# Kernel optimization log

Measured on AMD Instinct MI355X. Metric: run time of the kernel, lower is better.

Reference implementation:

```python
import jax, jax.numpy as jnp
import numpy as np

SEQ = 2048
D_MODEL = 2048
N_HEAD = 16
D_QK = 128
D_V = 128


def setup_inputs() -> dict:
    key = jax.random.key(0)
    ks = jax.random.split(key, 5)
    return {
        "x": jax.random.normal(ks[0], (SEQ, D_MODEL), dtype=jnp.float32),
        "q": jax.random.normal(ks[1], (N_HEAD, D_MODEL, D_QK), dtype=jnp.float32),
        "k": jax.random.normal(ks[2], (N_HEAD, D_MODEL, D_QK), dtype=jnp.float32),
        "v": jax.random.normal(ks[3], (N_HEAD, D_MODEL, D_V), dtype=jnp.float32),
        "o": jax.random.normal(ks[4], (N_HEAD, D_V, D_MODEL), dtype=jnp.float32),
        "theta_factor": jnp.asarray(10000.0, dtype=jnp.float32),
    }


def _rope_embed(x, theta_factor, d_qk):
    # x: [n_head, seq, d_qk]; faithful to source: rate is LINEAR in theta_factor
    seq = x.shape[1]
    d_rope = d_qk // 2
    rate = theta_factor * (-jnp.arange(d_rope, dtype=x.dtype) / d_rope)  # [d_rope]
    pos = jnp.arange(seq, dtype=x.dtype)                                 # [seq]
    rot = pos[:, None] * rate[None, :]                                   # [seq, d_rope]
    sin, cos = jnp.sin(rot), jnp.cos(rot)
    x1, x2 = x[..., :d_rope], x[..., d_rope:]
    y = jnp.concatenate([cos * x1 - sin * x2, sin * x1 + cos * x2], axis=-1)
    return y / d_qk ** 0.25  # qk_layer_norm is None path


def reference(x, q, k, v, o, theta_factor):
    seq, d_model = x.shape
    n_head, _, d_qk = q.shape
    d_v = v.shape[2]
    scale = 1.0 / jnp.sqrt(jnp.asarray(n_head * d_v * d_model, dtype=x.dtype))
    # causal mask: (tril - 1) * 1e9, as in source
    mask = (jnp.tril(jnp.ones((seq, seq), dtype=x.dtype)) - 1.0) * 1e9
    # per-head projections (vmapped heads expressed as einsum over h)
    rq = _rope_embed(jnp.einsum('sd,hde->hse', x, q), theta_factor, d_qk)
    rk = _rope_embed(jnp.einsum('sd,hde->hse', x, k), theta_factor, d_qk)
    vs = jnp.einsum('sd,hdv->hsv', x, v)
    scores = jnp.einsum('hse,hte->hst', rq, rk) + mask  # [h, s, s]
    w = jax.nn.softmax(scores, axis=-1)
    y = jnp.einsum('hst,htv->hsv', w, vs)
    z = jnp.einsum('hsv,hvd->sd', y, o)
    return z * scale
```

## Files before the change

kernel.cpp:

```cpp
#include <hip/hip_runtime.h>
#include <math.h>


typedef _Float16 half_t;
typedef __attribute__((ext_vector_type(8))) _Float16 half8;
typedef __attribute__((ext_vector_type(4))) float f32x4;

#define SEQ   2048
#define DM    2048
#define NHEAD 16

__device__ __forceinline__ f32x4 mfma16(half8 a, half8 b, f32x4 c) {
  return __builtin_amdgcn_mfma_f32_16x16x32_f16(a, b, c, 0, 0, 0);
}

__device__ __forceinline__ void gll16(const half_t* g, half_t* l) {
  __builtin_amdgcn_global_load_lds(
      (const __attribute__((address_space(1))) unsigned int*)g,
      (__attribute__((address_space(3))) unsigned int*)l, 16, 0, 0);
}

template <int CTRL>
__device__ __forceinline__ float dppf(float v) {
  int r = __builtin_amdgcn_mov_dpp(__builtin_bit_cast(int, v), CTRL, 0xF, 0xF,
                                   true);
  return __builtin_bit_cast(float, r);
}
__device__ __forceinline__ float red16_max(float v) {
  v = fmaxf(v, dppf<0xB1>(v));
  v = fmaxf(v, dppf<0x4E>(v));
  v = fmaxf(v, dppf<0x141>(v));
  v = fmaxf(v, dppf<0x140>(v));
  return v;
}
__device__ __forceinline__ float red16_sum(float v) {
  v += dppf<0xB1>(v);
  v += dppf<0x4E>(v);
  v += dppf<0x141>(v);
  v += dppf<0x140>(v);
  return v;
}

__device__ __forceinline__ void tpose32(const float* __restrict__ in,
                                        half_t* __restrict__ hi,
                                        half_t* __restrict__ lo, int R, int C,
                                        int r0, int c0, float (*tile)[33],
                                        int tid) {
  int tx = tid & 31, ty = tid >> 5;
#pragma unroll
  for (int i = 0; i < 32; i += 8)
    tile[ty + i][tx] = in[(size_t)(r0 + ty + i) * C + c0 + tx];
  __syncthreads();
#pragma unroll
  for (int i = 0; i < 32; i += 8) {
    float v = tile[tx][ty + i];
    half_t h = (half_t)v;
    size_t oidx = (size_t)(c0 + ty + i) * R + r0 + tx;
    hi[oidx] = h;
    if (lo) lo[oidx] = (half_t)(v - (float)h);
  }
}

__global__ __launch_bounds__(256)
void k_pre(const float* __restrict__ x, const float* __restrict__ q,
           const float* __restrict__ k, const float* __restrict__ v,
           const float* __restrict__ o, const float* __restrict__ thetap,
           half_t* __restrict__ Xh, half_t* __restrict__ Xl,
           half_t* __restrict__ WTh, half_t* __restrict__ WTl,
           half_t* __restrict__ VhT, half_t* __restrict__ OT,
           float2* __restrict__ trig) {
  __shared__ float tile[32][33];
  int b = blockIdx.x, tid = threadIdx.x;
  if (b < 4096) {
    int i = b * 256 + tid;
    float4 vv = ((const float4*)x)[i];
    union { half_t h[4]; uint2 u; } H, L;
    H.h[0] = (half_t)vv.x; H.h[1] = (half_t)vv.y;
    H.h[2] = (half_t)vv.z; H.h[3] = (half_t)vv.w;
    L.h[0] = (half_t)(vv.x - (float)H.h[0]);
    L.h[1] = (half_t)(vv.y - (float)H.h[1]);
    L.h[2] = (half_t)(vv.z - (float)H.h[2]);
    L.h[3] = (half_t)(vv.w - (float)H.h[3]);
    *(uint2*)&Xh[(size_t)i * 4] = H.u;
    *(uint2*)&Xl[(size_t)i * 4] = L.u;
  } else if (b < 16384) {
    int j = b - 4096;
    int which = j >> 12, z = (j >> 8) & 15, tb = j & 255;
    int c0 = (tb & 3) * 32, r0 = (tb >> 2) * 32;
    const float* src =
        (which == 0 ? q : which == 1 ? k : v) + (size_t)z * 2048 * 128;
    size_t doff = (size_t)z * 128 * 2048;
    if (which == 0)
      tpose32(src, WTh + doff, WTl + doff, 2048, 128, r0, c0, tile, tid);
    else if (which == 1) {
      size_t koff = (size_t)16 * 128 * 2048 + doff;
      tpose32(src, WTh + koff, WTl + koff, 2048, 128, r0, c0, tile, tid);
    } else
      tpose32(src, VhT + doff, nullptr, 2048, 128, r0, c0, tile, tid);
  } else if (b < 20480) {
    int j = b - 16384;
    int c0 = (j & 63) * 32, r0 = (j >> 6) * 32;
    tpose32(o, OT, nullptr, 2048, 2048, r0, c0, tile, tid);
  } else {
    int idx = (b - 20480) * 256 + tid;
    int s = idx >> 6, e = idx & 63;
    float th = thetap[0];
    float rate = th * (-(float)e * (1.0f / 64.0f));
    float rot = (float)s * rate;
    double rev = (double)rot * 0.15915494309189535;
    double fr = rev - rint(rev);
    float thr = (float)(fr * 6.283185307179586);
    float sn = sinf(thr), cs = cosf(thr);
    const float inv4 = 0.2973017787506803f;
    trig[idx] = make_float2(cs * inv4, sn * inv4);
  }
}

__global__ __launch_bounds__(256, 2)
void k_proj(const half_t* __restrict__ Xh, const half_t* __restrict__ Xl,
            const half_t* __restrict__ WTh, const half_t* __restrict__ WTl,
            const float2* __restrict__ trig, half_t* __restrict__ Rh,
            half_t* __restrict__ Rl) {
  __shared__ __align__(16) char smem[65536];
  half_t* sAh = (half_t*)smem;
  half_t* sAl = (half_t*)(smem + 16384);
  half_t* sBh = (half_t*)(smem + 32768);
  half_t* sBl = (half_t*)(smem + 49152);
  int y = blockIdx.y;
  int m0 = blockIdx.x * 128;
  const half_t* wth = WTh + (size_t)y * 128 * DM;
  const half_t* wtl = WTl + (size_t)y * 128 * DM;
  int lane = threadIdx.x & 63, wave = threadIdx.x >> 6;
  int l15 = lane & 15, quad = lane >> 4;
  int wm = wave >> 1, wn = wave & 1;

  f32x4 acc[4][4];
#pragma unroll
  for (int a = 0; a < 4; ++a)
#pragma unroll
    for (int b = 0; b < 4; ++b) acc[a][b] = (f32x4)0.0f;

  for (int kt = 0; kt < DM / 64; ++kt) {
    int k0 = kt * 64;
#pragma unroll
    for (int i = 0; i < 4; ++i) {
      int c = wave * 4 + i;
      int g = c * 64 + lane;
      int row = g >> 3;
      int lc = (g & 7) ^ (row & 7);
      size_t ro = (size_t)row * DM + k0 + lc * 8;
      gll16(Xh + (size_t)m0 * DM + ro, sAh + c * 512);
      gll16(Xl + (size_t)m0 * DM + ro, sAl + c * 512);
      gll16(wth + ro, sBh + c * 512);
      gll16(wtl + ro, sBl + c * 512);
    }
    __syncthreads();
#pragma unroll
    for (int kk = 0; kk < 2; ++kk) {
      half8 ah[4], al[4], bh[4], bl[4];
#pragma unroll
      for (int t = 0; t < 4; ++t) {
        int ar = wm * 64 + t * 16 + l15;
        int br = wn * 64 + t * 16 + l15;
        int ao = ar * 64 + (((kk * 4 + quad) ^ (ar & 7)) * 8);
        int bo = br * 64 + (((kk * 4 + quad) ^ (br & 7)) * 8);
        ah[t] = *(const half8*)&sAh[ao];
        al[t] = *(const half8*)&sAl[ao];
        bh[t] = *(const half8*)&sBh[bo];
        bl[t] = *(const half8*)&sBl[bo];
      }
#pragma unroll
      for (int im = 0; im < 4; ++im)
#pragma unroll
        for (int in = 0; in < 4; ++in) {
          acc[im][in] = mfma16(ah[im], bh[in], acc[im][in]);
          acc[im][in] = mfma16(ah[im], bl[in], acc[im][in]);
          acc[im][in] = mfma16(al[im], bh[in], acc[im][in]);
        }
    }
    __syncthreads();
  }
  float* tile = (float*)smem;
  size_t ybase = (size_t)y * SEQ * 128;
#pragma unroll
  for (int p = 0; p < 2; ++p) {
    if (p) __syncthreads();
    if (wm == p) {
#pragma unroll
      for (int im = 0; im < 4; ++im)
#pragma unroll
        for (int in = 0; in < 4; ++in)
#pragma unroll
          for (int r = 0; r < 4; ++r)
            tile[(im * 16 + quad * 4 + r) * 132 + wn * 64 + in * 16 + l15] =
                acc[im][in][r];
    }
    __syncthreads();
    int e = lane;
#pragma unroll 4
    for (int rr = 0; rr < 16; ++rr) {
      int rloc = wave * 16 + rr;
      int s = m0 + p * 64 + rloc;
      float x1 = tile[rloc * 132 + e];
      float x2 = tile[rloc * 132 + 64 + e];
      float2 sc = trig[s * 64 + e];
      float y1 = sc.x * x1 - sc.y * x2;
      float y2 = sc.y * x1 + sc.x * x2;
      half_t h1 = (half_t)y1, h2 = (half_t)y2;
      size_t base = ybase + (size_t)s * 128;
      Rh[base + e] = h1;       Rl[base + e] = (half_t)(y1 - (float)h1);
      Rh[base + 64 + e] = h2;  Rl[base + 64 + e] = (half_t)(y2 - (float)h2);
    }
  }
}

template <int HALF_OUT>
__global__ __launch_bounds__(256)
void k_gemm1(const half_t* __restrict__ A, const half_t* __restrict__ B,
             void* __restrict__ Cv, float scale) {
  __shared__ __align__(16) half_t sA[64 * 64], sB[128 * 64];
  int lin = blockIdx.y * 16 + blockIdx.x;
  int xcd = lin & 7, slot = lin >> 3;
  int bx = (xcd & 3) * 4 + (slot & 3);
  int by = (xcd >> 2) * 16 + (slot >> 2);
  int am0 = by * 64, bn0 = bx * 128;
  int lane = threadIdx.x & 63, wave = threadIdx.x >> 6;
  int l15 = lane & 15, quad = lane >> 4;
  int wm = wave >> 1, wn = wave & 1;

  f32x4 acc[2][4];
#pragma unroll
  for (int a = 0; a < 2; ++a)
#pragma unroll
    for (int b = 0; b < 4; ++b) acc[a][b] = (f32x4)0.0f;

  for (int kt = 0; kt < DM / 64; ++kt) {
    int k0 = kt * 64;
#pragma unroll
    for (int i = 0; i < 2; ++i) {
      int g0 = (i * 4 + wave) * 64;
      int g = g0 + lane;
      int row = g >> 3;
      int lc = (g & 7) ^ (row & 7);
      gll16(A + (size_t)(am0 + row) * 2048 + k0 + lc * 8, sA + g0 * 8);
    }
#pragma unroll
    for (int i = 0; i < 4; ++i) {
      int g0 = (i * 4 + wave) * 64;
      int g = g0 + lane;
      int row = g >> 3;
      int lc = (g & 7) ^ (row & 7);
      gll16(B + (size_t)(bn0 + row) * 2048 + k0 + lc * 8, sB + g0 * 8);
    }
    __syncthreads();
#pragma unroll
    for (int kk = 0; kk < 2; ++kk) {
      half8 ah[2], bh[4];
#pragma unroll
      for (int t = 0; t < 2; ++t) {
        int ar = wm * 32 + t * 16 + l15;
        ah[t] = *(const half8*)&sA[ar * 64 + (((kk * 4 + quad) ^ (ar & 7)) * 8)];
      }
#pragma unroll
      for (int t = 0; t < 4; ++t) {
        int br = wn * 64 + t * 16 + l15;
        bh[t] = *(const half8*)&sB[br * 64 + (((kk * 4 + quad) ^ (br & 7)) * 8)];
      }
#pragma unroll
      for (int im = 0; im < 2; ++im)
#pragma unroll
        for (int in = 0; in < 4; ++in)
          acc[im][in] = mfma16(ah[im], bh[in], acc[im][in]);
    }
    __syncthreads();
  }
#pragma unroll
  for (int im = 0; im < 2; ++im)
#pragma unroll
    for (int in = 0; in < 4; ++in)
#pragma unroll
      for (int r = 0; r < 4; ++r) {
        int row = am0 + wm * 32 + im * 16 + quad * 4 + r;
        int col = bn0 + wn * 64 + in * 16 + l15;
        if (HALF_OUT)
          ((half_t*)Cv)[(size_t)row * 2048 + col] = (half_t)(acc[im][in][r] * scale);
        else
          ((float*)Cv)[(size_t)row * 2048 + col] = acc[im][in][r] * scale;
      }
}

__global__ __launch_bounds__(256, 2)
void k_flash(const half_t* __restrict__ Rh, const half_t* __restrict__ Rl,
             const half_t* __restrict__ VST, half_t* __restrict__ Ybig) {
  int idx = blockIdx.x;
  int h = idx & 15;
  int qt = (idx < 256) ? (31 - (idx >> 4)) : ((idx - 256) >> 4);
  int lane = threadIdx.x & 63, wave = threadIdx.x >> 6;
  int l15 = lane & 15, quad = lane >> 4;

  const half_t* RQh = Rh + (size_t)h * SEQ * 128;
  const half_t* RQl = Rl + (size_t)h * SEQ * 128;
  const half_t* RKh = Rh + (size_t)(NHEAD + h) * SEQ * 128;
  const half_t* RKl = Rl + (size_t)(NHEAD + h) * SEQ * 128;
  const half_t* Vt  = VST + (size_t)h * 128 * SEQ;

  __shared__ __align__(16) half_t sKh[64 * 128];
  __shared__ __align__(16) half_t sKl[64 * 128];
  __shared__ __align__(16) half_t sVt[128 * 64];
  __shared__ __align__(16) half_t sP[64 * 72];

  int q0 = qt * 64;

  half8 qh[4], ql[4];
#pragma unroll
  for (int kk = 0; kk < 4; ++kk) {
    size_t ad = (size_t)(q0 + wave * 16 + l15) * 128 + kk * 32 + quad * 8;
    qh[kk] = *(const half8*)&RQh[ad];
    ql[kk] = *(const half8*)&RQl[ad];
  }

  float m_st[4], l_st[4];
  f32x4 oacc[8];
#pragma unroll
  for (int r = 0; r < 4; ++r) { m_st[r] = -INFINITY; l_st[r] = 0.0f; }
#pragma unroll
  for (int iv = 0; iv < 8; ++iv) oacc[iv] = (f32x4)0.0f;

  int nkb = qt + 1;
  for (int kb = 0; kb < nkb; ++kb) {
    int t0 = kb * 64;
#pragma unroll
    for (int i = 0; i < 4; ++i) {
      int c = wave * 4 + i;
      int rk = c * 4 + (lane >> 4);
      int ck = (lane & 15) ^ (rk & 15);
      gll16(RKh + (size_t)(t0 + rk) * 128 + ck * 8, sKh + c * 512);
      gll16(RKl + (size_t)(t0 + rk) * 128 + ck * 8, sKl + c * 512);
      int rv = c * 8 + (lane >> 3);
      int cv = (lane & 7) ^ (rv & 7);
      gll16(Vt + (size_t)rv * SEQ + t0 + cv * 8, sVt + c * 512);
    }
    __syncthreads();

    f32x4 sacc[4];
#pragma unroll
    for (int in = 0; in < 4; ++in) sacc[in] = (f32x4)0.0f;
#pragma unroll
    for (int kk = 0; kk < 4; ++kk)
#pragma unroll
      for (int in = 0; in < 4; ++in) {
        int bo = (in * 16 + l15) * 128 + (((kk * 4 + quad) ^ l15) * 8);
        half8 bh = *(const half8*)&sKh[bo];
        half8 bl = *(const half8*)&sKl[bo];
        sacc[in] = mfma16(qh[kk], bh, sacc[in]);
        sacc[in] = mfma16(qh[kk], bl, sacc[in]);
        sacc[in] = mfma16(ql[kk], bh, sacc[in]);
      }
    if (kb == qt) {
#pragma unroll
      for (int in = 0; in < 4; ++in)
#pragma unroll
        for (int r = 0; r < 4; ++r)
          if (in * 16 + l15 > wave * 16 + quad * 4 + r) sacc[in][r] = -1e30f;
    }
    float alpha[4];
#pragma unroll
    for (int r = 0; r < 4; ++r) {
      float mx = fmaxf(fmaxf(sacc[0][r], sacc[1][r]),
                       fmaxf(sacc[2][r], sacc[3][r]));
      mx = red16_max(mx);
      float mnew = fmaxf(m_st[r], mx);
      alpha[r] = __expf(m_st[r] - mnew);
      float sum = 0.0f;
#pragma unroll
      for (int in = 0; in < 4; ++in) {
        float p = __expf(sacc[in][r] - mnew);
        sacc[in][r] = p;
        sum += p;
      }
      sum = red16_sum(sum);
      l_st[r] = l_st[r] * alpha[r] + sum;
      m_st[r] = mnew;
    }
#pragma unroll
    for (int in = 0; in < 4; ++in)
#pragma unroll
      for (int r = 0; r < 4; ++r)
        sP[(wave * 16 + quad * 4 + r) * 72 + in * 16 + l15] =
            (half_t)sacc[in][r];
#pragma unroll
    for (int iv = 0; iv < 8; ++iv)
#pragma unroll
      for (int r = 0; r < 4; ++r) oacc[iv][r] *= alpha[r];

#pragma unroll
    for (int kk2 = 0; kk2 < 2; ++kk2) {
      half8 pa =
          *(const half8*)&sP[(wave * 16 + l15) * 72 + kk2 * 32 + quad * 8];
#pragma unroll
      for (int iv = 0; iv < 8; ++iv) {
        half8 vb = *(const half8*)&sVt[(iv * 16 + l15) * 64 +
                                       (((kk2 * 4 + quad) ^ (l15 & 7)) * 8)];
        oacc[iv] = mfma16(pa, vb, oacc[iv]);
      }
    }
    __syncthreads();
  }
  float invl[4];
#pragma unroll
  for (int r = 0; r < 4; ++r) invl[r] = 1.0f / l_st[r];
#pragma unroll
  for (int iv = 0; iv < 8; ++iv)
#pragma unroll
    for (int r = 0; r < 4; ++r) {
      int row = q0 + wave * 16 + quad * 4 + r;
      int col = h * 128 + iv * 16 + l15;
      Ybig[(size_t)row * 2048 + col] = (half_t)(oacc[iv][r] * invl[r]);
    }
}

extern "C" void kernel_launch(void* const* d_in, const int* in_sizes, int n_in,
                              void* d_out, int out_size, void* d_ws,
                              size_t ws_size, hipStream_t stream) {
  const float* x = (const float*)d_in[0];
  const float* q = (const float*)d_in[1];
  const float* k = (const float*)d_in[2];
  const float* v = (const float*)d_in[3];
  const float* o = (const float*)d_in[4];
  const float* theta = (const float*)d_in[5];
  float* out = (float*)d_out;

  char* ws = (char*)d_ws;
  const size_t HB = (size_t)2048 * 2048 * 2;
  half_t* Xh   = (half_t*)(ws);
  half_t* Xl   = (half_t*)(ws + HB);
  half_t* WTh  = (half_t*)(ws + 2 * HB);
  half_t* WTl  = (half_t*)(ws + 4 * HB);
  half_t* VhT  = (half_t*)(ws + 6 * HB);
  half_t* OT   = (half_t*)(ws + 7 * HB);
  half_t* Rh   = (half_t*)(ws + 8 * HB);
  half_t* Rl   = (half_t*)(ws + 10 * HB);
  float2* trig = (float2*)(ws + 12 * HB);
  half_t* VST  = (half_t*)(ws + 2 * HB);
  half_t* Ybig = (half_t*)(ws + 3 * HB);

  k_pre<<<20992, 256, 0, stream>>>(x, q, k, v, o, theta, Xh, Xl, WTh, WTl,
                                   VhT, OT, trig);
  k_proj<<<dim3(16, 32), 256, 0, stream>>>(Xh, Xl, WTh, WTl, trig, Rh, Rl);
  k_gemm1<1><<<dim3(16, 32), 256, 0, stream>>>(VhT, Xh, VST, 1.0f);
  k_flash<<<512, 256, 0, stream>>>(Rh, Rl, VST, Ybig);
  k_gemm1<0><<<dim3(16, 32), 256, 0, stream>>>(Ybig, OT, out, 1.0f / 2048.0f);
}
```

Baseline: 342.4 us.

## Double-buffer projection GEMM LDS tiles with K=32 stages and new swizzle

The projection GEMM's shared-memory staging changes from a single 64-wide K tile to two 32-wide K buffers. The next tile's global-to-LDS loads are issued while the current tile is computed, which cuts the barriers per iteration from two to one. The LDS swizzle is adjusted to the 32-element row layout. Each stage now does half the work, which may expose more barrier overhead, and there is a risk that the async global_load_lds has not completed at the barrier.

```diff
diff --git a/kernel.cpp b/kernel.cpp
--- a/kernel.cpp
+++ b/kernel.cpp
@@ -122,64 +122,78 @@
             const float2* __restrict__ trig, half_t* __restrict__ Rh,
             half_t* __restrict__ Rl) {
   __shared__ __align__(16) char smem[65536];
-  half_t* sAh = (half_t*)smem;
-  half_t* sAl = (half_t*)(smem + 16384);
-  half_t* sBh = (half_t*)(smem + 32768);
-  half_t* sBl = (half_t*)(smem + 49152);
   int y = blockIdx.y;
   int m0 = blockIdx.x * 128;
   const half_t* wth = WTh + (size_t)y * 128 * DM;
   const half_t* wtl = WTl + (size_t)y * 128 * DM;
+  const half_t* xh = Xh + (size_t)m0 * DM;
+  const half_t* xl = Xl + (size_t)m0 * DM;
   int lane = threadIdx.x & 63, wave = threadIdx.x >> 6;
   int l15 = lane & 15, quad = lane >> 4;
   int wm = wave >> 1, wn = wave & 1;
 
+  int c0s = wave * 2, c1s = wave * 2 + 1;
+  int rs0 = c0s * 16 + (lane >> 2);
+  int rs1 = c1s * 16 + (lane >> 2);
+  int sc0 = (lane & 3) ^ ((rs0 >> 1) & 3);
+  int sc1 = (lane & 3) ^ ((rs1 >> 1) & 3);
+  size_t go0 = (size_t)rs0 * DM + sc0 * 8;
+  size_t go1 = (size_t)rs1 * DM + sc1 * 8;
+
   f32x4 acc[4][4];
 #pragma unroll
   for (int a = 0; a < 4; ++a)
 #pragma unroll
     for (int b = 0; b < 4; ++b) acc[a][b] = (f32x4)0.0f;
 
-  for (int kt = 0; kt < DM / 64; ++kt) {
-    int k0 = kt * 64;
-#pragma unroll
-    for (int i = 0; i < 4; ++i) {
-      int c = wave * 4 + i;
-      int g = c * 64 + lane;
-      int row = g >> 3;
-      int lc = (g & 7) ^ (row & 7);
-      size_t ro = (size_t)row * DM + k0 + lc * 8;
-      gll16(Xh + (size_t)m0 * DM + ro, sAh + c * 512);
-      gll16(Xl + (size_t)m0 * DM + ro, sAl + c * 512);
-      gll16(wth + ro, sBh + c * 512);
-      gll16(wtl + ro, sBl + c * 512);
-    }
-    __syncthreads();
-#pragma unroll
-    for (int kk = 0; kk < 2; ++kk) {
-      half8 ah[4], al[4], bh[4], bl[4];
-#pragma unroll
-      for (int t = 0; t < 4; ++t) {
-        int ar = wm * 64 + t * 16 + l15;
-        int br = wn * 64 + t * 16 + l15;
-        int ao = ar * 64 + (((kk * 4 + quad) ^ (ar & 7)) * 8);
-        int bo = br * 64 + (((kk * 4 + quad) ^ (br & 7)) * 8);
-        ah[t] = *(const half8*)&sAh[ao];
-        al[t] = *(const half8*)&sAl[ao];
-        bh[t] = *(const half8*)&sBh[bo];
-        bl[t] = *(const half8*)&sBl[bo];
-      }
-#pragma unroll
-      for (int im = 0; im < 4; ++im)
-#pragma unroll
-        for (int in = 0; in < 4; ++in) {
-          acc[im][in] = mfma16(ah[im], bh[in], acc[im][in]);
-          acc[im][in] = mfma16(ah[im], bl[in], acc[im][in]);
-          acc[im][in] = mfma16(al[im], bh[in], acc[im][in]);
-        }
-    }
-    __syncthreads();
-  }
+  auto STAGE = [&](int k0, int b) {
+    half_t* sb = (half_t*)(smem + b * 32768);
+    gll16(xh + go0 + k0, sb + c0s * 512);
+    gll16(xh + go1 + k0, sb + c1s * 512);
+    gll16(xl + go0 + k0, sb + 4096 + c0s * 512);
+    gll16(xl + go1 + k0, sb + 4096 + c1s * 512);
+    gll16(wth + go0 + k0, sb + 8192 + c0s * 512);
+    gll16(wth + go1 + k0, sb + 8192 + c1s * 512);
+    gll16(wtl + go0 + k0, sb + 12288 + c0s * 512);
+    gll16(wtl + go1 + k0, sb + 12288 + c1s * 512);
+  };
+
+  auto COMPUTE = [&](int b) {
+    half_t* sb = (half_t*)(smem + b * 32768);
+    half8 ah[4], al[4], bh[4], bl[4];
+#pragma unroll
+    for (int t = 0; t < 4; ++t) {
+      int ar = wm * 64 + t * 16 + l15;
+      int ao = ar * 32 + ((quad ^ ((ar >> 1) & 3)) * 8);
+      ah[t] = *(const half8*)&sb[ao];
+      al[t] = *(const half8*)&sb[4096 + ao];
+      int br = wn * 64 + t * 16 + l15;
+      int bo = br * 32 + ((quad ^ ((br >> 1) & 3)) * 8);
+      bh[t] = *(const half8*)&sb[8192 + bo];
+      bl[t] = *(const half8*)&sb[12288 + bo];
+    }
+#pragma unroll
+    for (int im = 0; im < 4; ++im)
+#pragma unroll
+      for (int in = 0; in < 4; ++in) {
+        acc[im][in] = mfma16(ah[im], bh[in], acc[im][in]);
+        acc[im][in] = mfma16(ah[im], bl[in], acc[im][in]);
+        acc[im][in] = mfma16(al[im], bh[in], acc[im][in]);
+      }
+  };
+
+  STAGE(0, 0);
+  __syncthreads();
+  int cur = 0;
+  for (int kt = 0; kt < 63; ++kt) {
+    STAGE((kt + 1) * 32, cur ^ 1);
+    COMPUTE(cur);
+    __syncthreads();
+    cur ^= 1;
+  }
+  COMPUTE(cur);
+  __syncthreads();
+
   float* tile = (float*)smem;
   size_t ybase = (size_t)y * SEQ * 128;
 #pragma unroll
```

New measurement: 350.2 us. 2.3% more time.

## Prefetch next K/V tile into registers to overlap loads with attention compute

Applied to the files above, without the earlier changes.

The attention loop no longer uses direct global-to-LDS loads followed by a full sync. It now loads the next K-high, K-low and V tile into registers while the current tile is being computed, then writes them to LDS at the top of the next iteration. The full __syncthreads is replaced by an LDS-only wait plus a raw barrier. The aim is to hide global memory latency behind the MFMA work, at the cost of about 48 extra VGPRs per thread, which could reduce occupancy or cause spills.

```diff
diff --git a/kernel.cpp b/kernel.cpp
--- a/kernel.cpp
+++ b/kernel.cpp
@@ -319,6 +319,33 @@
     ql[kk] = *(const half8*)&RQl[ad];
   }
 
+  int rk_r = (lane >> 4);
+  int rv_r = (lane >> 3);
+  float4 pk[4], pl[4], pv[4];
+
+  auto FLOAD = [&](int t0, float4* k_, float4* l_, float4* v_) {
+#pragma unroll
+    for (int i = 0; i < 4; ++i) {
+      int c = wave * 4 + i;
+      int rk = c * 4 + rk_r;
+      int ck = (lane & 15) ^ (rk & 15);
+      k_[i] = *(const float4*)(RKh + (size_t)(t0 + rk) * 128 + ck * 8);
+      l_[i] = *(const float4*)(RKl + (size_t)(t0 + rk) * 128 + ck * 8);
+      int rv = c * 8 + rv_r;
+      int cv = (lane & 7) ^ (rv & 7);
+      v_[i] = *(const float4*)(Vt + (size_t)rv * SEQ + t0 + cv * 8);
+    }
+  };
+  auto FWRITE = [&](const float4* k_, const float4* l_, const float4* v_) {
+#pragma unroll
+    for (int i = 0; i < 4; ++i) {
+      int c = wave * 4 + i;
+      *(float4*)(sKh + c * 512 + lane * 8) = k_[i];
+      *(float4*)(sKl + c * 512 + lane * 8) = l_[i];
+      *(float4*)(sVt + c * 512 + lane * 8) = v_[i];
+    }
+  };
+
   float m_st[4], l_st[4];
   f32x4 oacc[8];
 #pragma unroll
@@ -327,20 +354,12 @@
   for (int iv = 0; iv < 8; ++iv) oacc[iv] = (f32x4)0.0f;
 
   int nkb = qt + 1;
+  FLOAD(0, pk, pl, pv);
   for (int kb = 0; kb < nkb; ++kb) {
-    int t0 = kb * 64;
-#pragma unroll
-    for (int i = 0; i < 4; ++i) {
-      int c = wave * 4 + i;
-      int rk = c * 4 + (lane >> 4);
-      int ck = (lane & 15) ^ (rk & 15);
-      gll16(RKh + (size_t)(t0 + rk) * 128 + ck * 8, sKh + c * 512);
-      gll16(RKl + (size_t)(t0 + rk) * 128 + ck * 8, sKl + c * 512);
-      int rv = c * 8 + (lane >> 3);
-      int cv = (lane & 7) ^ (rv & 7);
-      gll16(Vt + (size_t)rv * SEQ + t0 + cv * 8, sVt + c * 512);
-    }
-    __syncthreads();
+    FWRITE(pk, pl, pv);
+    if (kb + 1 < nkb) FLOAD((kb + 1) * 64, pk, pl, pv);
+    asm volatile("s_waitcnt lgkmcnt(0)" ::: "memory");
+    __builtin_amdgcn_s_barrier();
 
     f32x4 sacc[4];
 #pragma unroll
@@ -404,7 +423,8 @@
         oacc[iv] = mfma16(pa, vb, oacc[iv]);
       }
     }
-    __syncthreads();
+    asm volatile("" ::: "memory");
+    __builtin_amdgcn_s_barrier();
   }
   float invl[4];
 #pragma unroll
```

Result: slower. 389.6 us (+13.8%).

## Prefetch next K/V tile into registers to overlap loads with attention compute

Applied to the files above, without the earlier changes.

Replaces direct global-to-LDS loads of the K (hi/lo) and V tiles with register prefetch. The next block's tiles are loaded into registers while the current block is computed, then written to shared memory at the start of the next iteration. Barriers become raw s_barrier calls with explicit lgkmcnt waits. This is meant to hide global memory latency behind the MFMA work, at the cost of 12 extra float4 registers per thread, which could reduce occupancy.

```diff
diff --git a/kernel.cpp b/kernel.cpp
--- a/kernel.cpp
+++ b/kernel.cpp
@@ -319,6 +319,33 @@
     ql[kk] = *(const half8*)&RQl[ad];
   }
 
+  int rk_r = (lane >> 4);
+  int rv_r = (lane >> 3);
+
+  float4 pk0, pk1, pk2, pk3, pl0, pl1, pl2, pl3, pv0, pv1, pv2, pv3;
+
+#define FL_ONE(i, t0)                                                     \
+  {                                                                       \
+    int c = wave * 4 + i;                                                 \
+    int rk = c * 4 + rk_r;                                                \
+    int ck = (lane & 15) ^ (rk & 15);                                     \
+    pk##i = *(const float4*)(RKh + (size_t)((t0) + rk) * 128 + ck * 8);   \
+    pl##i = *(const float4*)(RKl + (size_t)((t0) + rk) * 128 + ck * 8);   \
+    int rv = c * 8 + rv_r;                                                \
+    int cv = (lane & 7) ^ (rv & 7);                                       \
+    pv##i = *(const float4*)(Vt + (size_t)rv * SEQ + (t0) + cv * 8);      \
+  }
+#define FLOAD(t0) FL_ONE(0, t0) FL_ONE(1, t0) FL_ONE(2, t0) FL_ONE(3, t0)
+
+#define FW_ONE(i)                                                         \
+  {                                                                       \
+    int c = wave * 4 + i;                                                 \
+    *(float4*)(sKh + c * 512 + lane * 8) = pk##i;                         \
+    *(float4*)(sKl + c * 512 + lane * 8) = pl##i;                         \
+    *(float4*)(sVt + c * 512 + lane * 8) = pv##i;                         \
+  }
+#define FWRITE() FW_ONE(0) FW_ONE(1) FW_ONE(2) FW_ONE(3)
+
   float m_st[4], l_st[4];
   f32x4 oacc[8];
 #pragma unroll
@@ -327,20 +354,12 @@
   for (int iv = 0; iv < 8; ++iv) oacc[iv] = (f32x4)0.0f;
 
   int nkb = qt + 1;
+  FLOAD(0);
   for (int kb = 0; kb < nkb; ++kb) {
-    int t0 = kb * 64;
-#pragma unroll
-    for (int i = 0; i < 4; ++i) {
-      int c = wave * 4 + i;
-      int rk = c * 4 + (lane >> 4);
-      int ck = (lane & 15) ^ (rk & 15);
-      gll16(RKh + (size_t)(t0 + rk) * 128 + ck * 8, sKh + c * 512);
-      gll16(RKl + (size_t)(t0 + rk) * 128 + ck * 8, sKl + c * 512);
-      int rv = c * 8 + (lane >> 3);
-      int cv = (lane & 7) ^ (rv & 7);
-      gll16(Vt + (size_t)rv * SEQ + t0 + cv * 8, sVt + c * 512);
-    }
-    __syncthreads();
+    FWRITE();
+    if (kb + 1 < nkb) FLOAD((kb + 1) * 64);
+    asm volatile("s_waitcnt lgkmcnt(0)" ::: "memory");
+    __builtin_amdgcn_s_barrier();
 
     f32x4 sacc[4];
 #pragma unroll
@@ -404,7 +423,8 @@
         oacc[iv] = mfma16(pa, vb, oacc[iv]);
       }
     }
-    __syncthreads();
+    asm volatile("" ::: "memory");
+    __builtin_amdgcn_s_barrier();
   }
   float invl[4];
 #pragma unroll
@@ -417,6 +437,10 @@
       int col = h * 128 + iv * 16 + l15;
       Ybig[(size_t)row * 2048 + col] = (half_t)(oacc[iv][r] * invl[r]);
     }
+#undef FL_ONE
+#undef FLOAD
+#undef FW_ONE
+#undef FWRITE
 }
 
 extern "C" void kernel_launch(void* const* d_in, const int* in_sizes, int n_in,
```

Measured after the change: 339.6 us. Within noise of the previous version (-0.8%).
